# Optimization experiments

Measured on AMD Instinct MI355X. Metric: run time of the kernel, lower is better.

Reference implementation:

```python
import jax, jax.numpy as jnp
import numpy as np

B, T, D, H = 2, 2048, 1024, 16
DK = D // H


def setup_inputs() -> dict:
    key = jax.random.key(0)
    ks = jax.random.split(key, 12)
    s = 1.0 / np.sqrt(D)
    inp = {
        "q_inp": jax.random.normal(ks[0], (B, T, D), jnp.float32),
        "k_inp": jax.random.normal(ks[1], (B, T, D), jnp.float32),
        "v_inp": jax.random.normal(ks[2], (B, T, D), jnp.float32),
        # causal mask: True = position is masked out
        "attn_mask": jnp.triu(jnp.ones((T, T), jnp.bool_), k=1),
        "Wq": jax.random.uniform(ks[3], (D, D), jnp.float32, -s, s),
        "bq": jax.random.uniform(ks[4], (D,), jnp.float32, -s, s),
        "Wk": jax.random.uniform(ks[5], (D, D), jnp.float32, -s, s),
        "bk": jax.random.uniform(ks[6], (D,), jnp.float32, -s, s),
        "Wv": jax.random.uniform(ks[7], (D, D), jnp.float32, -s, s),
        "bv": jax.random.uniform(ks[8], (D,), jnp.float32, -s, s),
        "Wo": jax.random.uniform(ks[9], (D, D), jnp.float32, -s, s),
        "bo": jax.random.uniform(ks[10], (D,), jnp.float32, -s, s),
    }
    return inp


def _split_heads(x):
    # [B,T,D] -> [B,H,T,DK]
    Bx, Tx, _ = x.shape
    return x.reshape(Bx, Tx, H, DK).transpose(0, 2, 1, 3)


def reference(q_inp, k_inp, v_inp, attn_mask, Wq, bq, Wk, bk, Wv, bv, Wo, bo):
    Q = _split_heads(q_inp @ Wq + bq)
    K = _split_heads(k_inp @ Wk + bk)
    V = _split_heads(v_inp @ Wv + bv)
    scale = 1.0 / jnp.sqrt(jnp.asarray(DK, Q.dtype))
    scores = jnp.einsum("bhqd,bhkd->bhqk", Q, K) * scale  # [B,H,T,T]
    scores = jnp.where(attn_mask, -jnp.inf, scores)
    attn = jax.nn.softmax(scores, axis=-1)  # dropout p=0 -> identity
    ctx = jnp.einsum("bhqk,bhkd->bhqd", attn, V)
    out = ctx.transpose(0, 2, 1, 3).reshape(B, T, D) @ Wo + bo
    return (out, attn)
```

## Files before the change

kernel.cpp:

```cpp
#include <hip/hip_runtime.h>
#include <hip/hip_bf16.h>
#include <math.h>


typedef unsigned short bfu;
typedef __attribute__((ext_vector_type(8))) short short8;
typedef __attribute__((ext_vector_type(4))) float f32x4;

#define AS1(p) ((const __attribute__((address_space(1))) void*)(p))
#define AS3(p) ((__attribute__((address_space(3))) void*)(p))
#define SOFT_C 16.0f

__device__ __forceinline__ void gld16(const void* g, void* l) {
  __builtin_amdgcn_global_load_lds(AS1(g), AS3(l), 16, 0, 0);
}

__device__ __forceinline__ bfu f2bf(float f) {
  unsigned int u = __float_as_uint(f);
  u = (u + 0x7fffu + ((u >> 16) & 1u)) >> 16;
  return (bfu)u;
}
__device__ __forceinline__ float bf2f(bfu b) {
  return __uint_as_float(((unsigned int)b) << 16);
}
__device__ __forceinline__ short8 lds_read8(const bfu* p) {
  return *reinterpret_cast<const short8*>(p);
}

__global__ __launch_bounds__(256) void cvt_x_kernel(
    const float* __restrict__ q, const float* __restrict__ k,
    const float* __restrict__ v, bfu* __restrict__ out) {
  size_t idx = ((size_t)blockIdx.x * 256 + threadIdx.x) * 8;
  const float* src; size_t off;
  if (idx < 4194304u)       { src = q; off = idx; }
  else if (idx < 8388608u)  { src = k; off = idx - 4194304u; }
  else                      { src = v; off = idx - 8388608u; }
  float4 a = *reinterpret_cast<const float4*>(src + off);
  float4 b = *reinterpret_cast<const float4*>(src + off + 4);
  short8 r;
  r[0] = (short)f2bf(a.x); r[1] = (short)f2bf(a.y);
  r[2] = (short)f2bf(a.z); r[3] = (short)f2bf(a.w);
  r[4] = (short)f2bf(b.x); r[5] = (short)f2bf(b.y);
  r[6] = (short)f2bf(b.z); r[7] = (short)f2bf(b.w);
  *reinterpret_cast<short8*>(out + idx) = r;
}

__global__ __launch_bounds__(256) void cvt_wt_kernel(
    const float* __restrict__ Wq, const float* __restrict__ Wk,
    const float* __restrict__ Wv, const float* __restrict__ Wo,
    bfu* __restrict__ Wt) {
  __shared__ float tile[32][33];
  const int z = blockIdx.z;
  const float* W = z == 0 ? Wq : z == 1 ? Wk : z == 2 ? Wv : Wo;
  bfu* out = Wt + (size_t)z * 1048576;
  const int n0 = blockIdx.x * 32, k0 = blockIdx.y * 32;
  const int tx = threadIdx.x, ty = threadIdx.y;
#pragma unroll
  for (int i = 0; i < 4; ++i)
    tile[ty + i * 8][tx] = W[(size_t)(k0 + ty + i * 8) * 1024 + n0 + tx];
  __syncthreads();
#pragma unroll
  for (int i = 0; i < 4; ++i)
    out[(size_t)(n0 + ty + i * 8) * 1024 + k0 + tx] = f2bf(tile[tx][ty + i * 8]);
}

template <int MODE>
__global__ __launch_bounds__(256) void gemm_bt_kernel(
    const bfu* __restrict__ Aall, const bfu* __restrict__ Btall,
    const float* __restrict__ bias0, const float* __restrict__ bias1,
    const float* __restrict__ bias2, bfu* __restrict__ outQKV,
    float* __restrict__ outF) {
  __shared__ bfu sA[128 * 64];
  __shared__ bfu sB[128 * 64];
  const int z = blockIdx.z;
  const int m0 = blockIdx.x * 128, n0 = blockIdx.y * 128;
  const bfu* A = Aall + (size_t)z * 4194304;
  const bfu* Bt = Btall + (size_t)z * 1048576;
  const float* bias = (z == 0) ? bias0 : (z == 1 ? bias1 : bias2);
  const int tid = threadIdx.x, w = tid >> 6, l = tid & 63;
  const int quad = l >> 4, lane16 = l & 15;
  const int l7 = lane16 & 7;
  const int mb = (w >> 1) * 64, nb = (w & 1) * 64;

  f32x4 acc[4][4] = {};

  for (int kt = 0; kt < 16; ++kt) {
    const int k0 = kt * 64;
    __syncthreads();
#pragma unroll
    for (int j = 0; j < 4; ++j) {
      const int chunk = (w * 4 + j) * 64 + l;
      const int row = chunk >> 3, c = (chunk & 7) ^ (row & 7);
      gld16(A + (size_t)(m0 + row) * 1024 + k0 + c * 8, sA + chunk * 8);
      gld16(Bt + (size_t)(n0 + row) * 1024 + k0 + c * 8, sB + chunk * 8);
    }
    __syncthreads();
#pragma unroll
    for (int ks = 0; ks < 2; ++ks) {
      const int cf = ((ks * 4 + quad) ^ l7) * 8;
      short8 af[4], bfr[4];
#pragma unroll
      for (int x = 0; x < 4; ++x) {
        af[x]  = lds_read8(sA + (mb + x * 16 + lane16) * 64 + cf);
        bfr[x] = lds_read8(sB + (nb + x * 16 + lane16) * 64 + cf);
      }
#pragma unroll
      for (int mi = 0; mi < 4; ++mi)
#pragma unroll
        for (int ni = 0; ni < 4; ++ni)
          acc[mi][ni] = __builtin_amdgcn_mfma_f32_16x16x32_bf16(
              af[mi], bfr[ni], acc[mi][ni], 0, 0, 0);
    }
  }

#pragma unroll
  for (int ni = 0; ni < 4; ++ni) {
    const int n = n0 + nb + ni * 16 + lane16;
    const float bv = bias[n];
#pragma unroll
    for (int mi = 0; mi < 4; ++mi) {
#pragma unroll
      for (int r = 0; r < 4; ++r) {
        const int m = m0 + mb + mi * 16 + quad * 4 + r;
        float v = acc[mi][ni][r] + bv;
        if (MODE == 0) {
          if (z == 0) v *= 0.125f;
          const int b = m >> 11, t = m & 2047;
          const int h = n >> 6, dk = n & 63;
          outQKV[(size_t)z * 4194304 +
                 (((size_t)(b * 16 + h) * 2048 + t) * 64 + dk)] = f2bf(v);
        } else {
          outF[(size_t)m * 1024 + n] = v;
        }
      }
    }
  }
}

__global__ __launch_bounds__(256) void vt_kernel(const bfu* __restrict__ V,
                                                 bfu* __restrict__ vT) {
  __shared__ bfu sT[64][72];
  const int bh = blockIdx.y, t0 = blockIdx.x * 64;
  const int tid = threadIdx.x;
  const bfu* src = V + (size_t)bh * 131072 + (size_t)t0 * 64;
#pragma unroll
  for (int j = 0; j < 2; ++j) {
    const int ch = j * 256 + tid;
    const int row = ch >> 3, c = ch & 7;
    short8 v = *reinterpret_cast<const short8*>(src + row * 64 + c * 8);
#pragma unroll
    for (int e = 0; e < 8; ++e) sT[c * 8 + e][row] = (bfu)v[e];
  }
  __syncthreads();
#pragma unroll
  for (int j = 0; j < 2; ++j) {
    const int ch = j * 256 + tid;
    const int d = ch >> 3, c = ch & 7;
    short8 o = lds_read8(&sT[d][c * 8]);
    *reinterpret_cast<short8*>(vT + (size_t)bh * 131072 + (size_t)d * 2048 +
                               t0 + c * 8) = o;
  }
}

__global__ __launch_bounds__(256) void attn_kernel(
    const bfu* __restrict__ qkv, const bfu* __restrict__ vT,
    float* __restrict__ attnO, bfu* __restrict__ ctx) {
  __shared__ bfu sK[2][64 * 64];
  __shared__ bfu sVt[2][64 * 64];
  __shared__ bfu sP[128 * 72];
  const int bh = blockIdx.y;
  const int iq = (bh & 16) ? (int)blockIdx.x : 15 - (int)blockIdx.x;
  const int tid = threadIdx.x, w = tid >> 6, l = tid & 63;
  const int quad = l >> 4, lane16 = l & 15;
  const int l7 = lane16 & 7;
  const bfu* Qb = qkv + ((size_t)bh * 2048 + iq * 128) * 64;
  const bfu* Kb = qkv + 4194304 + (size_t)bh * 131072;
  const bfu* VTb = vT + (size_t)bh * 131072;
  float* attnRow = attnO + (size_t)bh * 4194304 + (size_t)iq * 128 * 2048;

  short8 aq[2][2];
#pragma unroll
  for (int mf = 0; mf < 2; ++mf)
#pragma unroll
    for (int ks = 0; ks < 2; ++ks)
      aq[mf][ks] = *reinterpret_cast<const short8*>(
          Qb + (size_t)(w * 32 + mf * 16 + lane16) * 64 + (ks * 4 + quad) * 8);

  const int jmax = 2 * iq + 1;
  const int wrow0 = iq * 128 + w * 32;
  const int jmaxw = (wrow0 + 31) >> 6;

  float esum[2][4] = {};

#pragma unroll
  for (int j = 0; j < 2; ++j) {
    const int chunk = (w * 2 + j) * 64 + l;
    const int row = chunk >> 3, c = (chunk & 7) ^ (row & 7);
    gld16(Kb + row * 64 + c * 8, sK[0] + chunk * 8);
  }
  __syncthreads();
  int cur = 0;
  for (int jj = 0; jj <= jmax; ++jj) {
    if (jj < jmax) {
#pragma unroll
      for (int j = 0; j < 2; ++j) {
        const int chunk = (w * 2 + j) * 64 + l;
        const int row = chunk >> 3, c = (chunk & 7) ^ (row & 7);
        gld16(Kb + (size_t)(jj + 1) * 4096 + row * 64 + c * 8,
              sK[cur ^ 1] + chunk * 8);
      }
    }
    if (jj <= jmaxw) {
      f32x4 s[2][4] = {};
      __builtin_amdgcn_s_setprio(1);
#pragma unroll
      for (int ks = 0; ks < 2; ++ks) {
        const int cf = ((ks * 4 + quad) ^ l7) * 8;
        short8 kb[4];
#pragma unroll
        for (int nf = 0; nf < 4; ++nf)
          kb[nf] = lds_read8(sK[cur] + (nf * 16 + lane16) * 64 + cf);
#pragma unroll
        for (int mf = 0; mf < 2; ++mf)
#pragma unroll
          for (int nf = 0; nf < 4; ++nf)
            s[mf][nf] = __builtin_amdgcn_mfma_f32_16x16x32_bf16(
                aq[mf][ks], kb[nf], s[mf][nf], 0, 0, 0);
      }
      __builtin_amdgcn_s_setprio(0);
      if (jj * 64 + 63 > wrow0) {
#pragma unroll
        for (int mf = 0; mf < 2; ++mf)
#pragma unroll
          for (int nf = 0; nf < 4; ++nf)
#pragma unroll
            for (int r = 0; r < 4; ++r) {
              const int qg = wrow0 + mf * 16 + quad * 4 + r;
              const int kg = jj * 64 + nf * 16 + lane16;
              if (kg > qg) s[mf][nf][r] = -INFINITY;
            }
      }
#pragma unroll
      for (int mf = 0; mf < 2; ++mf)
#pragma unroll
        for (int r = 0; r < 4; ++r) {
          float a = __expf(s[mf][0][r] - SOFT_C) + __expf(s[mf][1][r] - SOFT_C);
          float b = __expf(s[mf][2][r] - SOFT_C) + __expf(s[mf][3][r] - SOFT_C);
          esum[mf][r] += a + b;
        }
    }
    __syncthreads();
    cur ^= 1;
  }
  float linv[2][4];
#pragma unroll
  for (int mf = 0; mf < 2; ++mf)
#pragma unroll
    for (int r = 0; r < 4; ++r) {
      float e = esum[mf][r];
      e += __shfl_xor(e, 1, 64);
      e += __shfl_xor(e, 2, 64);
      e += __shfl_xor(e, 4, 64);
      e += __shfl_xor(e, 8, 64);
      linv[mf][r] = 1.f / e;
    }

  f32x4 o[2][4] = {};
#pragma unroll
  for (int j = 0; j < 2; ++j) {
    const int chunk = (w * 2 + j) * 64 + l;
    const int row = chunk >> 3, c = (chunk & 7) ^ (row & 7);
    gld16(Kb + row * 64 + c * 8, sK[0] + chunk * 8);
    gld16(VTb + (size_t)row * 2048 + c * 8, sVt[0] + chunk * 8);
  }
  __syncthreads();
  cur = 0;
  for (int jj = 0; jj <= jmax; ++jj) {
    if (jj < jmax) {
#pragma unroll
      for (int j = 0; j < 2; ++j) {
        const int chunk = (w * 2 + j) * 64 + l;
        const int row = chunk >> 3, c = (chunk & 7) ^ (row & 7);
        gld16(Kb + (size_t)(jj + 1) * 4096 + row * 64 + c * 8,
              sK[cur ^ 1] + chunk * 8);
        gld16(VTb + (size_t)row * 2048 + (jj + 1) * 64 + c * 8,
              sVt[cur ^ 1] + chunk * 8);
      }
    }
    if (jj <= jmaxw) {
      f32x4 s[2][4] = {};
      __builtin_amdgcn_s_setprio(1);
#pragma unroll
      for (int ks = 0; ks < 2; ++ks) {
        const int cf = ((ks * 4 + quad) ^ l7) * 8;
        short8 kb[4];
#pragma unroll
        for (int nf = 0; nf < 4; ++nf)
          kb[nf] = lds_read8(sK[cur] + (nf * 16 + lane16) * 64 + cf);
#pragma unroll
        for (int mf = 0; mf < 2; ++mf)
#pragma unroll
          for (int nf = 0; nf < 4; ++nf)
            s[mf][nf] = __builtin_amdgcn_mfma_f32_16x16x32_bf16(
                aq[mf][ks], kb[nf], s[mf][nf], 0, 0, 0);
      }
      __builtin_amdgcn_s_setprio(0);
      if (jj * 64 + 63 > wrow0) {
#pragma unroll
        for (int mf = 0; mf < 2; ++mf)
#pragma unroll
          for (int nf = 0; nf < 4; ++nf)
#pragma unroll
            for (int r = 0; r < 4; ++r) {
              const int qg = wrow0 + mf * 16 + quad * 4 + r;
              const int kg = jj * 64 + nf * 16 + lane16;
              if (kg > qg) s[mf][nf][r] = -INFINITY;
            }
      }
#pragma unroll
      for (int mf = 0; mf < 2; ++mf)
#pragma unroll
        for (int nf = 0; nf < 4; ++nf)
#pragma unroll
          for (int r = 0; r < 4; ++r) {
            const float p = __expf(s[mf][nf][r] - SOFT_C) * linv[mf][r];
            sP[(w * 32 + mf * 16 + quad * 4 + r) * 72 + nf * 16 + lane16] =
                f2bf(p);
          }
      __builtin_amdgcn_s_setprio(1);
#pragma unroll
      for (int ks = 0; ks < 2; ++ks) {
        const int cf = ((ks * 4 + quad) ^ l7) * 8;
        short8 ap[2], vb[4];
        ap[0] = lds_read8(sP + (w * 32 + lane16) * 72 + ks * 32 + quad * 8);
        ap[1] = lds_read8(sP + (w * 32 + 16 + lane16) * 72 + ks * 32 + quad * 8);
#pragma unroll
        for (int nf = 0; nf < 4; ++nf)
          vb[nf] = lds_read8(sVt[cur] + (nf * 16 + lane16) * 64 + cf);
#pragma unroll
        for (int mf = 0; mf < 2; ++mf)
#pragma unroll
          for (int nf = 0; nf < 4; ++nf)
            o[mf][nf] = __builtin_amdgcn_mfma_f32_16x16x32_bf16(
                ap[mf], vb[nf], o[mf][nf], 0, 0, 0);
      }
      __builtin_amdgcn_s_setprio(0);
#pragma unroll
      for (int it = 0; it < 4; ++it) {
        const int lin = it * 64 + l;
        const int row = lin >> 3, ch = (lin & 7) * 8;
        short8 pv = lds_read8(sP + (w * 32 + row) * 72 + ch);
        float4 f0, f1;
        f0.x = bf2f((bfu)pv[0]); f0.y = bf2f((bfu)pv[1]);
        f0.z = bf2f((bfu)pv[2]); f0.w = bf2f((bfu)pv[3]);
        f1.x = bf2f((bfu)pv[4]); f1.y = bf2f((bfu)pv[5]);
        f1.z = bf2f((bfu)pv[6]); f1.w = bf2f((bfu)pv[7]);
        float* gp = attnRow + (size_t)(w * 32 + row) * 2048 + jj * 64 + ch;
        *reinterpret_cast<float4*>(gp) = f0;
        *reinterpret_cast<float4*>(gp + 4) = f1;
      }
    }
    __syncthreads();
    cur ^= 1;
  }

  {
    const int colz = (jmaxw + 1) * 64;
    const int nz4 = (2048 - colz) >> 2;
    const float4 z4 = {0.f, 0.f, 0.f, 0.f};
    for (int r = 0; r < 32; ++r) {
      float* rp = attnRow + (size_t)(w * 32 + r) * 2048 + colz;
      for (int c = l; c < nz4; c += 64) reinterpret_cast<float4*>(rp)[c] = z4;
    }
  }

  __syncthreads();
#pragma unroll
  for (int mf = 0; mf < 2; ++mf)
#pragma unroll
    for (int nf = 0; nf < 4; ++nf)
#pragma unroll
      for (int r = 0; r < 4; ++r)
        sP[(w * 32 + mf * 16 + quad * 4 + r) * 72 + nf * 16 + lane16] =
            f2bf(o[mf][nf][r]);
  __syncthreads();
  const int b = bh >> 4, h = bh & 15;
#pragma unroll
  for (int it = 0; it < 4; ++it) {
    const int lin = it * 256 + tid;
    const int row = lin >> 3, ch = (lin & 7) * 8;
    short8 v = lds_read8(sP + row * 72 + ch);
    *reinterpret_cast<short8*>(
        ctx + ((size_t)(b * 2048 + iq * 128 + row)) * 1024 + h * 64 + ch) = v;
  }
}

extern "C" void kernel_launch(void* const* d_in, const int* in_sizes, int n_in,
                              void* d_out, int out_size, void* d_ws,
                              size_t ws_size, hipStream_t stream) {
  const float* q_inp = (const float*)d_in[0];
  const float* k_inp = (const float*)d_in[1];
  const float* v_inp = (const float*)d_in[2];
  const float* Wq = (const float*)d_in[4];
  const float* bq = (const float*)d_in[5];
  const float* Wk = (const float*)d_in[6];
  const float* bk = (const float*)d_in[7];
  const float* Wv = (const float*)d_in[8];
  const float* bv = (const float*)d_in[9];
  const float* Wo = (const float*)d_in[10];
  const float* bo = (const float*)d_in[11];

  bfu* X   = (bfu*)d_ws;
  bfu* Wt  = X + 12582912;
  bfu* qkv = Wt + 4194304;
  bfu* ctx = qkv + 12582912;
  bfu* vT  = X;
  float* out  = (float*)d_out;
  float* attn = out + 4194304;

  cvt_x_kernel<<<6144, 256, 0, stream>>>(q_inp, k_inp, v_inp, X);
  cvt_wt_kernel<<<dim3(32, 32, 4), dim3(32, 8), 0, stream>>>(Wq, Wk, Wv, Wo, Wt);
  gemm_bt_kernel<0><<<dim3(32, 8, 3), 256, 0, stream>>>(X, Wt, bq, bk, bv, qkv,
                                                        nullptr);
  vt_kernel<<<dim3(32, 32), 256, 0, stream>>>(qkv + 8388608, vT);
  attn_kernel<<<dim3(16, 32), 256, 0, stream>>>(qkv, vT, attn, ctx);
  gemm_bt_kernel<1><<<dim3(32, 8, 1), 256, 0, stream>>>(ctx, Wt + 3 * 1048576,
                                                        bo, bo, bo, nullptr, out);
}
```

Measured before the change: 760.9 us.

## Split attention into 64-row tiles with paired causal halves per block

Each block now processes two 64-row query tiles (tile x and tile 31-x) in sequence instead of one 128-row tile, so every block does the same total causal work. Each wave handles 16 rows instead of 32. The block-to-(bh,tile) mapping is also remapped so that concurrently scheduled blocks spread across heads for better K/V cache locality. The cost is less register reuse of K/V tiles per MFMA, since each loaded K/V tile now feeds only half as many query rows.

Result: no change. 749.2 us (-1.5%).

```diff
diff --git a/kernel.cpp b/kernel.cpp
--- a/kernel.cpp
+++ b/kernel.cpp
@@ -167,51 +167,50 @@
     float* __restrict__ attnO, bfu* __restrict__ ctx) {
   __shared__ bfu sK[2][64 * 64];
   __shared__ bfu sVt[2][64 * 64];
-  __shared__ bfu sP[128 * 72];
-  const int bh = blockIdx.y;
-  const int iq = (bh & 16) ? (int)blockIdx.x : 15 - (int)blockIdx.x;
+  __shared__ bfu sP[64 * 72];
+  const int linear = (int)blockIdx.y * 16 + (int)blockIdx.x;
+  const int bh = (linear & 7) * 4 + (linear >> 7);
+  const int x  = (linear >> 3) & 15;
   const int tid = threadIdx.x, w = tid >> 6, l = tid & 63;
   const int quad = l >> 4, lane16 = l & 15;
   const int l7 = lane16 & 7;
-  const bfu* Qb = qkv + ((size_t)bh * 2048 + iq * 128) * 64;
   const bfu* Kb = qkv + 4194304 + (size_t)bh * 131072;
   const bfu* VTb = vT + (size_t)bh * 131072;
-  float* attnRow = attnO + (size_t)bh * 4194304 + (size_t)iq * 128 * 2048;
-
-  short8 aq[2][2];
-#pragma unroll
-  for (int mf = 0; mf < 2; ++mf)
+  const int b = bh >> 4, h = bh & 15;
+
+#pragma unroll 1
+  for (int half = 0; half < 2; ++half) {
+    const int si = half ? (31 - x) : x;
+    const bfu* Qb = qkv + ((size_t)bh * 2048 + si * 64) * 64;
+    float* attnRow = attnO + (size_t)bh * 4194304 + (size_t)si * 64 * 2048;
+
+    short8 aq[2];
 #pragma unroll
     for (int ks = 0; ks < 2; ++ks)
-      aq[mf][ks] = *reinterpret_cast<const short8*>(
-          Qb + (size_t)(w * 32 + mf * 16 + lane16) * 64 + (ks * 4 + quad) * 8);
-
-  const int jmax = 2 * iq + 1;
-  const int wrow0 = iq * 128 + w * 32;
-  const int jmaxw = (wrow0 + 31) >> 6;
-
-  float esum[2][4] = {};
-
-#pragma unroll
-  for (int j = 0; j < 2; ++j) {
-    const int chunk = (w * 2 + j) * 64 + l;
-    const int row = chunk >> 3, c = (chunk & 7) ^ (row & 7);
-    gld16(Kb + row * 64 + c * 8, sK[0] + chunk * 8);
-  }
-  __syncthreads();
-  int cur = 0;
-  for (int jj = 0; jj <= jmax; ++jj) {
-    if (jj < jmax) {
-#pragma unroll
-      for (int j = 0; j < 2; ++j) {
-        const int chunk = (w * 2 + j) * 64 + l;
-        const int row = chunk >> 3, c = (chunk & 7) ^ (row & 7);
-        gld16(Kb + (size_t)(jj + 1) * 4096 + row * 64 + c * 8,
-              sK[cur ^ 1] + chunk * 8);
-      }
-    }
-    if (jj <= jmaxw) {
-      f32x4 s[2][4] = {};
+      aq[ks] = *reinterpret_cast<const short8*>(
+          Qb + (size_t)(w * 16 + lane16) * 64 + (ks * 4 + quad) * 8);
+
+    float esum[4] = {};
+
+#pragma unroll
+    for (int j = 0; j < 2; ++j) {
+      const int chunk = (w * 2 + j) * 64 + l;
+      const int row = chunk >> 3, c = (chunk & 7) ^ (row & 7);
+      gld16(Kb + row * 64 + c * 8, sK[0] + chunk * 8);
+    }
+    __syncthreads();
+    int cur = 0;
+    for (int jj = 0; jj <= si; ++jj) {
+      if (jj < si) {
+#pragma unroll
+        for (int j = 0; j < 2; ++j) {
+          const int chunk = (w * 2 + j) * 64 + l;
+          const int row = chunk >> 3, c = (chunk & 7) ^ (row & 7);
+          gld16(Kb + (size_t)(jj + 1) * 4096 + row * 64 + c * 8,
+                sK[cur ^ 1] + chunk * 8);
+        }
+      }
+      f32x4 s[4] = {};
       __builtin_amdgcn_s_setprio(1);
 #pragma unroll
       for (int ks = 0; ks < 2; ++ks) {
@@ -221,74 +220,64 @@
         for (int nf = 0; nf < 4; ++nf)
           kb[nf] = lds_read8(sK[cur] + (nf * 16 + lane16) * 64 + cf);
 #pragma unroll
-        for (int mf = 0; mf < 2; ++mf)
-#pragma unroll
-          for (int nf = 0; nf < 4; ++nf)
-            s[mf][nf] = __builtin_amdgcn_mfma_f32_16x16x32_bf16(
-                aq[mf][ks], kb[nf], s[mf][nf], 0, 0, 0);
+        for (int nf = 0; nf < 4; ++nf)
+          s[nf] = __builtin_amdgcn_mfma_f32_16x16x32_bf16(aq[ks], kb[nf],
+                                                          s[nf], 0, 0, 0);
       }
       __builtin_amdgcn_s_setprio(0);
-      if (jj * 64 + 63 > wrow0) {
-#pragma unroll
-        for (int mf = 0; mf < 2; ++mf)
-#pragma unroll
-          for (int nf = 0; nf < 4; ++nf)
-#pragma unroll
-            for (int r = 0; r < 4; ++r) {
-              const int qg = wrow0 + mf * 16 + quad * 4 + r;
-              const int kg = jj * 64 + nf * 16 + lane16;
-              if (kg > qg) s[mf][nf][r] = -INFINITY;
-            }
-      }
-#pragma unroll
-      for (int mf = 0; mf < 2; ++mf)
-#pragma unroll
-        for (int r = 0; r < 4; ++r) {
-          float a = __expf(s[mf][0][r] - SOFT_C) + __expf(s[mf][1][r] - SOFT_C);
-          float b = __expf(s[mf][2][r] - SOFT_C) + __expf(s[mf][3][r] - SOFT_C);
-          esum[mf][r] += a + b;
-        }
-    }
-    __syncthreads();
-    cur ^= 1;
-  }
-  float linv[2][4];
-#pragma unroll
-  for (int mf = 0; mf < 2; ++mf)
+      if (jj == si) {
+#pragma unroll
+        for (int nf = 0; nf < 4; ++nf)
+#pragma unroll
+          for (int r = 0; r < 4; ++r) {
+            const int qg = w * 16 + quad * 4 + r;
+            const int kg = nf * 16 + lane16;
+            if (kg > qg) s[nf][r] = -INFINITY;
+          }
+      }
+#pragma unroll
+      for (int r = 0; r < 4; ++r) {
+        float a = __expf(s[0][r] - SOFT_C) + __expf(s[1][r] - SOFT_C);
+        float b2 = __expf(s[2][r] - SOFT_C) + __expf(s[3][r] - SOFT_C);
+        esum[r] += a + b2;
+      }
+      __syncthreads();
+      cur ^= 1;
+    }
+    float linv[4];
 #pragma unroll
     for (int r = 0; r < 4; ++r) {
-      float e = esum[mf][r];
+      float e = esum[r];
       e += __shfl_xor(e, 1, 64);
       e += __shfl_xor(e, 2, 64);
       e += __shfl_xor(e, 4, 64);
       e += __shfl_xor(e, 8, 64);
-      linv[mf][r] = 1.f / e;
-    }
-
-  f32x4 o[2][4] = {};
-#pragma unroll
-  for (int j = 0; j < 2; ++j) {
-    const int chunk = (w * 2 + j) * 64 + l;
-    const int row = chunk >> 3, c = (chunk & 7) ^ (row & 7);
-    gld16(Kb + row * 64 + c * 8, sK[0] + chunk * 8);
-    gld16(VTb + (size_t)row * 2048 + c * 8, sVt[0] + chunk * 8);
-  }
-  __syncthreads();
-  cur = 0;
-  for (int jj = 0; jj <= jmax; ++jj) {
-    if (jj < jmax) {
-#pragma unroll
-      for (int j = 0; j < 2; ++j) {
-        const int chunk = (w * 2 + j) * 64 + l;
-        const int row = chunk >> 3, c = (chunk & 7) ^ (row & 7);
-        gld16(Kb + (size_t)(jj + 1) * 4096 + row * 64 + c * 8,
-              sK[cur ^ 1] + chunk * 8);
-        gld16(VTb + (size_t)row * 2048 + (jj + 1) * 64 + c * 8,
-              sVt[cur ^ 1] + chunk * 8);
-      }
-    }
-    if (jj <= jmaxw) {
-      f32x4 s[2][4] = {};
+      linv[r] = 1.f / e;
+    }
+
+    f32x4 o[4] = {};
+#pragma unroll
+    for (int j = 0; j < 2; ++j) {
+      const int chunk = (w * 2 + j) * 64 + l;
+      const int row = chunk >> 3, c = (chunk & 7) ^ (row & 7);
+      gld16(Kb + row * 64 + c * 8, sK[0] + chunk * 8);
+      gld16(VTb + (size_t)row * 2048 + c * 8, sVt[0] + chunk * 8);
+    }
+    __syncthreads();
+    cur = 0;
+    for (int jj = 0; jj <= si; ++jj) {
+      if (jj < si) {
+#pragma unroll
+        for (int j = 0; j < 2; ++j) {
+          const int chunk = (w * 2 + j) * 64 + l;
+          const int row = chunk >> 3, c = (chunk & 7) ^ (row & 7);
+          gld16(Kb + (size_t)(jj + 1) * 4096 + row * 64 + c * 8,
+                sK[cur ^ 1] + chunk * 8);
+          gld16(VTb + (size_t)row * 2048 + (jj + 1) * 64 + c * 8,
+                sVt[cur ^ 1] + chunk * 8);
+        }
+      }
+      f32x4 s[4] = {};
       __builtin_amdgcn_s_setprio(1);
 #pragma unroll
       for (int ks = 0; ks < 2; ++ks) {
@@ -298,100 +287,86 @@
         for (int nf = 0; nf < 4; ++nf)
           kb[nf] = lds_read8(sK[cur] + (nf * 16 + lane16) * 64 + cf);
 #pragma unroll
-        for (int mf = 0; mf < 2; ++mf)
-#pragma unroll
-          for (int nf = 0; nf < 4; ++nf)
-            s[mf][nf] = __builtin_amdgcn_mfma_f32_16x16x32_bf16(
-                aq[mf][ks], kb[nf], s[mf][nf], 0, 0, 0);
+        for (int nf = 0; nf < 4; ++nf)
+          s[nf] = __builtin_amdgcn_mfma_f32_16x16x32_bf16(aq[ks], kb[nf],
+                                                          s[nf], 0, 0, 0);
       }
       __builtin_amdgcn_s_setprio(0);
-      if (jj * 64 + 63 > wrow0) {
-#pragma unroll
-        for (int mf = 0; mf < 2; ++mf)
-#pragma unroll
-          for (int nf = 0; nf < 4; ++nf)
-#pragma unroll
-            for (int r = 0; r < 4; ++r) {
-              const int qg = wrow0 + mf * 16 + quad * 4 + r;
-              const int kg = jj * 64 + nf * 16 + lane16;
-              if (kg > qg) s[mf][nf][r] = -INFINITY;
-            }
-      }
-#pragma unroll
-      for (int mf = 0; mf < 2; ++mf)
+      if (jj == si) {
 #pragma unroll
         for (int nf = 0; nf < 4; ++nf)
 #pragma unroll
           for (int r = 0; r < 4; ++r) {
-            const float p = __expf(s[mf][nf][r] - SOFT_C) * linv[mf][r];
-            sP[(w * 32 + mf * 16 + quad * 4 + r) * 72 + nf * 16 + lane16] =
-                f2bf(p);
+            const int qg = w * 16 + quad * 4 + r;
+            const int kg = nf * 16 + lane16;
+            if (kg > qg) s[nf][r] = -INFINITY;
           }
+      }
+#pragma unroll
+      for (int nf = 0; nf < 4; ++nf)
+#pragma unroll
+        for (int r = 0; r < 4; ++r) {
+          const float p = __expf(s[nf][r] - SOFT_C) * linv[r];
+          sP[(w * 16 + quad * 4 + r) * 72 + nf * 16 + lane16] = f2bf(p);
+        }
       __builtin_amdgcn_s_setprio(1);
 #pragma unroll
       for (int ks = 0; ks < 2; ++ks) {
         const int cf = ((ks * 4 + quad) ^ l7) * 8;
-        short8 ap[2], vb[4];
-        ap[0] = lds_read8(sP + (w * 32 + lane16) * 72 + ks * 32 + quad * 8);
-        ap[1] = lds_read8(sP + (w * 32 + 16 + lane16) * 72 + ks * 32 + quad * 8);
+        short8 ap, vb[4];
+        ap = lds_read8(sP + (w * 16 + lane16) * 72 + ks * 32 + quad * 8);
 #pragma unroll
         for (int nf = 0; nf < 4; ++nf)
           vb[nf] = lds_read8(sVt[cur] + (nf * 16 + lane16) * 64 + cf);
 #pragma unroll
-        for (int mf = 0; mf < 2; ++mf)
-#pragma unroll
-          for (int nf = 0; nf < 4; ++nf)
-            o[mf][nf] = __builtin_amdgcn_mfma_f32_16x16x32_bf16(
-                ap[mf], vb[nf], o[mf][nf], 0, 0, 0);
+        for (int nf = 0; nf < 4; ++nf)
+          o[nf] = __builtin_amdgcn_mfma_f32_16x16x32_bf16(ap, vb[nf], o[nf],
+                                                          0, 0, 0);
       }
       __builtin_amdgcn_s_setprio(0);
 #pragma unroll
-      for (int it = 0; it < 4; ++it) {
+      for (int it = 0; it < 2; ++it) {
         const int lin = it * 64 + l;
         const int row = lin >> 3, ch = (lin & 7) * 8;
-        short8 pv = lds_read8(sP + (w * 32 + row) * 72 + ch);
+        short8 pv = lds_read8(sP + (w * 16 + row) * 72 + ch);
         float4 f0, f1;
         f0.x = bf2f((bfu)pv[0]); f0.y = bf2f((bfu)pv[1]);
         f0.z = bf2f((bfu)pv[2]); f0.w = bf2f((bfu)pv[3]);
         f1.x = bf2f((bfu)pv[4]); f1.y = bf2f((bfu)pv[5]);
         f1.z = bf2f((bfu)pv[6]); f1.w = bf2f((bfu)pv[7]);
-        float* gp = attnRow + (size_t)(w * 32 + row) * 2048 + jj * 64 + ch;
+        float* gp = attnRow + (size_t)(w * 16 + row) * 2048 + jj * 64 + ch;
         *reinterpret_cast<float4*>(gp) = f0;
         *reinterpret_cast<float4*>(gp + 4) = f1;
       }
-    }
-    __syncthreads();
-    cur ^= 1;
-  }
-
-  {
-    const int colz = (jmaxw + 1) * 64;
-    const int nz4 = (2048 - colz) >> 2;
-    const float4 z4 = {0.f, 0.f, 0.f, 0.f};
-    for (int r = 0; r < 32; ++r) {
-      float* rp = attnRow + (size_t)(w * 32 + r) * 2048 + colz;
-      for (int c = l; c < nz4; c += 64) reinterpret_cast<float4*>(rp)[c] = z4;
-    }
-  }
-
-  __syncthreads();
-#pragma unroll
-  for (int mf = 0; mf < 2; ++mf)
+      __syncthreads();
+      cur ^= 1;
+    }
+
+    {
+      const int colz = (si + 1) * 64;
+      const int nz4 = (2048 - colz) >> 2;
+      const float4 z4 = {0.f, 0.f, 0.f, 0.f};
+      for (int r = 0; r < 16; ++r) {
+        float* rp = attnRow + (size_t)(w * 16 + r) * 2048 + colz;
+        for (int c = l; c < nz4; c += 64) reinterpret_cast<float4*>(rp)[c] = z4;
+      }
+    }
+
 #pragma unroll
     for (int nf = 0; nf < 4; ++nf)
 #pragma unroll
       for (int r = 0; r < 4; ++r)
-        sP[(w * 32 + mf * 16 + quad * 4 + r) * 72 + nf * 16 + lane16] =
-            f2bf(o[mf][nf][r]);
-  __syncthreads();
-  const int b = bh >> 4, h = bh & 15;
-#pragma unroll
-  for (int it = 0; it < 4; ++it) {
-    const int lin = it * 256 + tid;
-    const int row = lin >> 3, ch = (lin & 7) * 8;
-    short8 v = lds_read8(sP + row * 72 + ch);
-    *reinterpret_cast<short8*>(
-        ctx + ((size_t)(b * 2048 + iq * 128 + row)) * 1024 + h * 64 + ch) = v;
+        sP[(w * 16 + quad * 4 + r) * 72 + nf * 16 + lane16] = f2bf(o[nf][r]);
+    __syncthreads();
+#pragma unroll
+    for (int it = 0; it < 2; ++it) {
+      const int lin = it * 256 + tid;
+      const int row = lin >> 3, ch = (lin & 7) * 8;
+      short8 v = lds_read8(sP + row * 72 + ch);
+      *reinterpret_cast<short8*>(
+          ctx + ((size_t)(b * 2048 + si * 64 + row)) * 1024 + h * 64 + ch) = v;
+    }
+    __syncthreads();
   }
 }
 
```
